# Kernel tuning notes

Hardware: AMD Instinct MI355X
Metric: run time of the kernel (lower is better)

## Reference

```python
import jax, jax.numpy as jnp
import numpy as np

V, D, H = 50000, 256, 4
HD = H * D            # concat head dim (TransformerConv concat=True)
HH, O = 256, 256      # invariant_hidden_dim, invariant_out_dim
B, N, E, L, A = 16, 1000, 4000, 64, 128
PAD = 0
SCALE = 1.0 / float(np.sqrt(D))


def emb_lookup(table, idx):
    # nn.Embedding with padding_idx: forward is a plain gather; grad at pad row is zeroed.
    rows = table[idx]
    return jnp.where((idx == PAD)[..., None], jax.lax.stop_gradient(rows), rows)


def transformer_conv(x, edge_index, ea, Wq, bq, Wk, bk, Wv, bv, We, Wskip, bskip):
    # PyG TransformerConv, heads=H, concat=True, root_weight=True, beta=False, dropout=0 (eval)
    n = x.shape[0]
    src, dst = edge_index[0], edge_index[1]
    q = (x @ Wq + bq).reshape(n, H, D)
    e = (ea @ We).reshape(-1, H, D)          # lin_edge (bias=False)
    k = (x @ Wk + bk).reshape(n, H, D)[src] + e
    v = (x @ Wv + bv).reshape(n, H, D)[src] + e
    alpha = (q[dst] * k).sum(-1) * SCALE      # [E,H]
    amax = jax.ops.segment_max(alpha, dst, num_segments=n)
    ex = jnp.exp(alpha - amax[dst])
    denom = jax.ops.segment_sum(ex, dst, num_segments=n)
    w = ex / denom[dst]                       # per-target-node softmax over incoming edges
    agg = jax.ops.segment_sum(v * w[..., None], dst, num_segments=n)
    return agg.reshape(n, HD) + x @ Wskip + bskip  # lin_skip on root


def mixed_embed(tok, node, graph_repr, emb):
    fixed = emb_lookup(emb, tok)
    flex = jnp.take_along_axis(graph_repr, node[..., None], axis=1)
    flex = jnp.where((node == PAD)[..., None], jax.lax.stop_gradient(flex), flex)
    return fixed + flex


def gru_last(xs, W_ih, W_hh, b_ih, b_hh):
    # torch nn.GRU, batch_first, 1 layer; only last hidden state is used
    gx = jnp.einsum('blh,gh->blg', xs, W_ih) + b_ih  # [B,L,3O]

    def step(h, g):
        gh = h @ W_hh.T + b_hh
        xr, xz, xn = jnp.split(g, 3, axis=-1)
        hr, hz, hn = jnp.split(gh, 3, axis=-1)
        r = jax.nn.sigmoid(xr + hr)
        z = jax.nn.sigmoid(xz + hz)
        c = jnp.tanh(xn + r * hn)
        return (1.0 - z) * c + z * h, None

    h0 = jnp.zeros((xs.shape[0], W_hh.shape[1]), xs.dtype)
    h_last, _ = jax.lax.scan(step, h0, jnp.swapaxes(gx, 0, 1))
    return h_last


def setup_inputs() -> dict:
    key = jax.random.key(0)
    ks = jax.random.split(key, 40)
    f = lambda i, shape, s=0.05: jax.random.normal(ks[i], shape, jnp.float32) * s
    ri = lambda i, shape, hi: jax.random.randint(ks[i], shape, 0, hi)
    return {
        'node_tokens': ri(0, (B, N), V),
        'edge_tokens': ri(1, (B, E), V),
        'edge_index': ri(2, (B, 2, E), N),
        'inv_token': ri(3, (B, L), V),
        'inv_node': ri(4, (B, L), N),
        'aa_token': ri(5, (B, A), V),
        'aa_node': ri(6, (B, A), N),
        'action_mask': jnp.ones((B, A), jnp.float32),
        'emb': f(7, (V, D), 0.02),
        'Wq': f(8, (D, HD)), 'bq': f(9, (HD,)),
        'Wk': f(10, (D, HD)), 'bk': f(11, (HD,)),
        'Wv': f(12, (D, HD)), 'bv': f(13, (HD,)),
        'We': f(14, (D, HD)),
        'Wskip': f(15, (D, HD)), 'bskip': f(16, (HD,)),
        'W1': f(17, (HD, D)), 'b1': f(18, (D,)),
        'Wp': f(19, (D, HH)), 'bp': f(20, (HH,)),
        'W_ih': f(21, (3 * O, HH)), 'W_hh': f(22, (3 * O, O)),
        'b_ih': f(23, (3 * O,)), 'b_hh': f(24, (3 * O,)),
        'Wab': f(25, (D, 1)), 'bab': f(26, (1,)),
        'Wap': f(27, (D, O)), 'bap': f(28, (O,)),
    }


def reference(node_tokens, edge_tokens, edge_index, inv_token, inv_node, aa_token, aa_node,
              action_mask, emb, Wq, bq, Wk, bk, Wv, bv, We, Wskip, bskip, W1, b1,
              Wp, bp, W_ih, W_hh, b_ih, b_hh, Wab, bab, Wap, bap):
    x = emb_lookup(emb, node_tokens)    # [B,N,D]
    ea = emb_lookup(emb, edge_tokens)   # [B,E,D]
    conv = jax.vmap(lambda xx, ei, ee: transformer_conv(
        xx, ei, ee, Wq, bq, Wk, bk, Wv, bv, We, Wskip, bskip))
    h = jax.nn.relu(conv(x, edge_index, ea))            # [B,N,HD]
    graph_repr = jax.nn.relu(h @ W1 + b1)               # [B,N,D]
    inv_h = jax.nn.relu(mixed_embed(inv_token, inv_node, graph_repr, emb) @ Wp + bp)
    inv = gru_last(inv_h, W_ih, W_hh, b_ih, b_hh)       # [B,O]
    aa_emb = mixed_embed(aa_token, aa_node, graph_repr, emb)  # [B,A,D]
    scores = jnp.einsum('bao,bo->ba', aa_emb @ Wap + bap, inv) + (aa_emb @ Wab + bab)[..., 0]
    inf_mask = jnp.maximum(jnp.log(action_mask), jnp.float32(np.finfo(np.float32).min))
    return scores + inf_mask
```

## Files before the change

### kernel.cpp

```cpp
#include <hip/hip_runtime.h>
#include <hip/hip_bf16.h>
#include <float.h>
#include <math.h>

typedef __hip_bfloat16 bf16;

#define B_ 16
#define N_ 1000
#define E_ 4000
#define L_ 64
#define A_ 128
#define D_ 256
#define H_ 4
#define HD_ 1024
#define SCALE_ 0.0625f

typedef __attribute__((ext_vector_type(8))) short short8;
typedef __attribute__((ext_vector_type(4))) float f32x4;

union U4S8 { uint4 u; short8 s; };

__device__ __forceinline__ unsigned short f2bf(float f) {
    bf16 h = __float2bfloat16(f);
    return *reinterpret_cast<unsigned short*>(&h);
}
__device__ __forceinline__ unsigned pack2(float a, float b) {
    return (unsigned)f2bf(a) | ((unsigned)f2bf(b) << 16);
}
__device__ __forceinline__ unsigned short rne1(float a) {
    unsigned ua = __float_as_uint(a);
    ua += 0x7fff + ((ua >> 16) & 1);
    return (unsigned short)(ua >> 16);
}
__device__ __forceinline__ float bflo(unsigned u) { return __uint_as_float(u << 16); }
__device__ __forceinline__ float bfhi(unsigned u) { return __uint_as_float(u & 0xffff0000u); }

#define LOG2E 1.4426950408889634f
__device__ __forceinline__ float fsigm(float x) {
    return __builtin_amdgcn_rcpf(1.f + __builtin_amdgcn_exp2f(-LOG2E * x));
}
__device__ __forceinline__ float ftanh(float x) {
    return 1.f - 2.f * __builtin_amdgcn_rcpf(1.f + __builtin_amdgcn_exp2f(2.f * LOG2E * x));
}

__global__ void convemb_kernel(const float* __restrict__ src, bf16* __restrict__ dst, long n4)
{
    long i = (long)blockIdx.x * 256 + threadIdx.x;
    if (i >= n4) return;
    float4 v = *(const float4*)(src + i * 4);
    *(uint2*)(dst + i * 4) = make_uint2(pack2(v.x, v.y), pack2(v.z, v.w));
}

__global__ void pack_all_kernel(const float* __restrict__ Wq, const float* __restrict__ Wk,
                                const float* __restrict__ Wv, const float* __restrict__ Wskip,
                                const float* __restrict__ We, const float* __restrict__ W1,
                                const float* __restrict__ Wp, const float* __restrict__ W_ih,
                                const float* __restrict__ Wap, const float* __restrict__ W_hh,
                                const float* __restrict__ bq, const float* __restrict__ bk,
                                const float* __restrict__ bv, const float* __restrict__ bskip,
                                unsigned* __restrict__ qkvsP, unsigned* __restrict__ WeP,
                                unsigned* __restrict__ W1P, unsigned* __restrict__ WpP,
                                unsigned* __restrict__ WihP, unsigned* __restrict__ WapP,
                                unsigned* __restrict__ WeTP,
                                short8* __restrict__ WhhP, float* __restrict__ bias4096)
{
    int i = blockIdx.x * 256 + threadIdx.x;
    if (i < 524288) {
        int k2 = i >> 12, n = i & 4095;
        const float* s = (n < 1024) ? Wq : (n < 2048) ? Wk : (n < 3072) ? Wv : Wskip;
        int col = n & 1023;
        qkvsP[i] = pack2(s[(long)(2 * k2) * 1024 + col], s[(long)(2 * k2 + 1) * 1024 + col]);
        return;
    }
    i -= 524288;
    if (i < 131072) {
        int k2 = i >> 10, n = i & 1023;
        WeP[i] = pack2(We[(long)(2 * k2) * 1024 + n], We[(long)(2 * k2 + 1) * 1024 + n]);
        return;
    }
    i -= 131072;
    if (i < 131072) {
        int k2 = i >> 8, n = i & 255;
        W1P[i] = pack2(W1[(long)(2 * k2) * 256 + n], W1[(long)(2 * k2 + 1) * 256 + n]);
        return;
    }
    i -= 131072;
    if (i < 32768) {
        int k2 = i >> 8, n = i & 255;
        WpP[i] = pack2(Wp[(long)(2 * k2) * 256 + n], Wp[(long)(2 * k2 + 1) * 256 + n]);
        return;
    }
    i -= 32768;
    if (i < 98304) {
        int k2 = i / 768, n = i % 768;
        WihP[i] = pack2(W_ih[(long)n * 256 + 2 * k2], W_ih[(long)n * 256 + 2 * k2 + 1]);
        return;
    }
    i -= 98304;
    if (i < 32768) {
        int k2 = i >> 8, n = i & 255;
        WapP[i] = pack2(Wap[(long)(2 * k2) * 256 + n], Wap[(long)(2 * k2 + 1) * 256 + n]);
        return;
    }
    i -= 32768;
    if (i < 131072) {
        int k2 = i >> 10, n = i & 1023;
        int d = n & 255, hb = n & ~255;
        WeTP[i] = pack2(We[(long)d * 1024 + hb + 2 * k2],
                        We[(long)d * 1024 + hb + 2 * k2 + 1]);
        return;
    }
    i -= 131072;
    if (i < 24576) {
        int lane = i & 63, tk = (i >> 6) & 7, tile = i >> 9;
        int n = tile * 16 + (lane & 15);
        const float* wp = W_hh + (long)n * 256 + tk * 32 + (lane >> 4) * 8;
        float4 w0 = *(const float4*)wp;
        float4 w1 = *(const float4*)(wp + 4);
        U4S8 u;
        u.u = make_uint4(pack2(w0.x, w0.y), pack2(w0.z, w0.w),
                         pack2(w1.x, w1.y), pack2(w1.z, w1.w));
        WhhP[i] = u.s;
        return;
    }
    i -= 24576;
    if (i < 4096) {
        int q = i >> 10, c = i & 1023;
        bias4096[i] = ((q == 0) ? bq : (q == 1) ? bk : (q == 2) ? bv : bskip)[c];
    }
}
#define PACK_ALL_TOT (524288 + 131072 + 131072 + 32768 + 98304 + 32768 + 131072 + 24576 + 4096)

__global__ void gxt_kernel(const bf16* __restrict__ gxh, bf16* __restrict__ gxT)
{
    int i = blockIdx.x * 256 + threadIdx.x;
    if (i >= B_ * L_ * 768) return;
    int b = i / (L_ * 768);
    int rem = i - b * (L_ * 768);
    int t = rem / 768, n = rem - (rem / 768) * 768;
    gxT[((long)t * 768 + n) * 16 + b] = gxh[i];
}

#define TM 128
#define TN 128
#define TK 32
#define ASTR 40
#define BSTR 132

template <typename CT>
__global__ __launch_bounds__(256)
void pgemm_kernel(const bf16* __restrict__ A, const int* __restrict__ arows,
                  const unsigned* __restrict__ Bp, const float* __restrict__ bias,
                  CT* __restrict__ C, int M, int K, int Nc, int relu_out,
                  long astride, int aoff, int colbase, int hslice, int addC)
{
    __shared__ short    As[TM * ASTR];
    __shared__ unsigned Bs[(TK / 2) * BSTR];

    const int tid  = threadIdx.x;
    const int lane = tid & 63;
    const int wave = tid >> 6;
    const int wm = wave >> 1, wn = wave & 1;
    const int quad = lane >> 4, c16 = lane & 15;
    const long row0 = (long)blockIdx.y * TM;
    const int  col0 = colbase + blockIdx.x * TN;
    const int  aoff2 = aoff + (hslice ? (col0 & ~255) : 0);

    const int sm  = tid >> 1;
    const int sh  = (tid & 1) * 16;
    const int sn2 = tid & 63;
    const int skk = (tid >> 6) * 4;

    long gr_row = row0 + sm;
    if (gr_row > M - 1) gr_row = M - 1;
    long ar = arows ? (long)arows[gr_row] : gr_row;
    const short* Arow = (const short*)A + ar * astride + aoff2 + sh;

    f32x4 acc[4][4];
    #pragma unroll
    for (int i = 0; i < 4; ++i)
        #pragma unroll
        for (int j = 0; j < 4; ++j)
            acc[i][j] = (f32x4){0.f, 0.f, 0.f, 0.f};

    for (int k0 = 0; k0 < K; k0 += TK) {
        {
            const short* p = Arow + k0;
            uint4 a = *(const uint4*)(p);
            uint4 b = *(const uint4*)(p + 8);
            *(uint4*)&As[sm * ASTR + sh]     = a;
            *(uint4*)&As[sm * ASTR + sh + 8] = b;
        }
        #pragma unroll
        for (int i = 0; i < 4; ++i) {
            int kk2 = skk + i;
            *(uint2*)&Bs[kk2 * BSTR + sn2 * 2] =
                *(const uint2*)&Bp[(long)(k0 / 2 + kk2) * Nc + col0 + sn2 * 2];
        }
        __syncthreads();

        short8 af[4];
        U4S8   bfr[4];
        #pragma unroll
        for (int mi = 0; mi < 4; ++mi) {
            int m = wm * 64 + mi * 16 + c16;
            af[mi] = *(const short8*)&As[m * ASTR + quad * 8];
        }
        #pragma unroll
        for (int ni = 0; ni < 4; ++ni) {
            int n = wn * 64 + ni * 16 + c16;
            uint4 u;
            u.x = Bs[(quad * 4 + 0) * BSTR + n];
            u.y = Bs[(quad * 4 + 1) * BSTR + n];
            u.z = Bs[(quad * 4 + 2) * BSTR + n];
            u.w = Bs[(quad * 4 + 3) * BSTR + n];
            bfr[ni].u = u;
        }
        #pragma unroll
        for (int mi = 0; mi < 4; ++mi)
            #pragma unroll
            for (int ni = 0; ni < 4; ++ni)
                acc[mi][ni] = __builtin_amdgcn_mfma_f32_16x16x32_bf16(
                    af[mi], bfr[ni].s, acc[mi][ni], 0, 0, 0);
        __syncthreads();
    }

    #pragma unroll
    for (int ni = 0; ni < 4; ++ni) {
        int col = col0 + wn * 64 + ni * 16 + c16;
        float bv = bias ? bias[col] : 0.f;
        #pragma unroll
        for (int mi = 0; mi < 4; ++mi) {
            long row = row0 + wm * 64 + mi * 16 + quad * 4;
            #pragma unroll
            for (int r = 0; r < 4; ++r) {
                if (row + r >= M) continue;
                float v = acc[mi][ni][r] + bv;
                if (addC) v += (float)C[(row + r) * Nc + col];
                if (relu_out) v = fmaxf(v, 0.f);
                C[(row + r) * Nc + col] = (CT)v;
            }
        }
    }
}

__global__ void zero_int_kernel(int* __restrict__ p, int n)
{
    int i = blockIdx.x * 256 + threadIdx.x;
    if (i < n) p[i] = 0;
}

__global__ void count_kernel(const int* __restrict__ edge_index, int b0,
                             int* __restrict__ cnt, int cE)
{
    int i = blockIdx.x * 256 + threadIdx.x;
    if (i >= cE) return;
    int bl = i / E_, ei = i % E_;
    int dst = edge_index[(long)(b0 + bl) * 2 * E_ + E_ + ei];
    atomicAdd(&cnt[bl * N_ + dst], 1);
}

__global__ __launch_bounds__(1024)
void scan_kernel(const int* __restrict__ cnt, int* __restrict__ row_start,
                 int* __restrict__ cursor)
{
    int bl = blockIdx.x;
    int tid = threadIdx.x;
    __shared__ int s[1024];
    int v = (tid < N_) ? cnt[bl * N_ + tid] : 0;
    s[tid] = v;
    __syncthreads();
    for (int off = 1; off < 1024; off <<= 1) {
        int t = (tid >= off) ? s[tid - off] : 0;
        __syncthreads();
        s[tid] += t;
        __syncthreads();
    }
    if (tid < N_) {
        int excl = s[tid] - v;
        row_start[bl * N_ + tid] = excl;
        cursor[bl * N_ + tid] = excl;
    }
}

__global__ void scatter_kernel(const int* __restrict__ edge_index, int b0,
                               int* __restrict__ cursor, int* __restrict__ elist, int cE)
{
    int i = blockIdx.x * 256 + threadIdx.x;
    if (i >= cE) return;
    int bl = i / E_, ei = i % E_;
    int dst = edge_index[(long)(b0 + bl) * 2 * E_ + E_ + ei];
    int pos = atomicAdd(&cursor[bl * N_ + dst], 1);
    elist[bl * E_ + pos] = ei;
}

__device__ __forceinline__ float d2(unsigned a, unsigned b)
{
    return bflo(a) * bflo(b) + bfhi(a) * bfhi(b);
}

__global__ void alpha_ex_kernel(const bf16* __restrict__ qkvs, const bf16* __restrict__ qWb,
                                const bf16* __restrict__ embh, const int* __restrict__ edge_tokens,
                                const int* __restrict__ edge_index,
                                int b0, float* __restrict__ ex, int cE)
{
    int eidx = blockIdx.x * 4 + (threadIdx.x >> 6);
    int l = threadIdx.x & 63;
    int bl = eidx / E_, ei = eidx % E_;
    const int* eb = edge_index + (long)(b0 + bl) * 2 * E_;
    int src = eb[ei], dst = eb[E_ + ei];
    int tok = edge_tokens[(long)(b0 + bl) * E_ + ei];
    int head = l >> 4;
    int li = l & 15;
    int joff = head * 256 + li * 16;

    const uint4* qp = (const uint4*)(qkvs + (long)(bl * N_ + dst) * 4096 + joff);
    const uint4* kp = (const uint4*)(qkvs + (long)(bl * N_ + src) * 4096 + 1024 + joff);
    const uint4* wp = (const uint4*)(qWb + (long)(bl * N_ + dst) * 1024 + joff);
    const uint4* xp = (const uint4*)(embh + (long)tok * 256 + li * 16);

    uint4 qa = qp[0], qb2 = qp[1];
    uint4 ka = kp[0], kb2 = kp[1];
    uint4 wa = wp[0], wb2 = wp[1];
    uint4 xa = xp[0], xb2 = xp[1];

    float s = d2(qa.x, ka.x) + d2(qa.y, ka.y) + d2(qa.z, ka.z) + d2(qa.w, ka.w)
            + d2(qb2.x, kb2.x) + d2(qb2.y, kb2.y) + d2(qb2.z, kb2.z) + d2(qb2.w, kb2.w)
            + d2(wa.x, xa.x) + d2(wa.y, xa.y) + d2(wa.z, xa.z) + d2(wa.w, xa.w)
            + d2(wb2.x, xb2.x) + d2(wb2.y, xb2.y) + d2(wb2.z, xb2.z) + d2(wb2.w, xb2.w);

    s += __shfl_down(s, 8);
    s += __shfl_down(s, 4);
    s += __shfl_down(s, 2);
    s += __shfl_down(s, 1);

    if (li == 0)
        ex[(long)head * cE + eidx] = __builtin_amdgcn_exp2f(s * (SCALE_ * LOG2E));
}

__global__ void agg_node_kernel(const bf16* __restrict__ qkvs, const bf16* __restrict__ embh,
                                const int* __restrict__ edge_tokens,
                                const float* __restrict__ ex, const int* __restrict__ edge_index,
                                const int* __restrict__ row_start, const int* __restrict__ cnt,
                                const int* __restrict__ elist,
                                int b0, int cE, bf16* __restrict__ aggb,
                                bf16* __restrict__ xsumb)
{
    int base = blockIdx.x;
    int bl = base / N_;
    int tid = threadIdx.x;
    int h = tid >> 6;
    int j0 = tid * 4;
    int jx = (tid & 63) * 4;

    int start = row_start[base];
    int deg = cnt[base];
    const int* el = elist + (long)bl * E_;
    const float* exh = ex + (long)h * cE;
    const int* srcp = edge_index + (long)(b0 + bl) * 2 * E_;
    const int* tokp = edge_tokens + (long)(b0 + bl) * E_;

    float d = 0.f;
    for (int t = 0; t < deg; ++t)
        d += exh[(long)bl * E_ + el[start + t]];
    float invd = (deg > 0) ? 1.f / d : 0.f;

    float a0 = 0.f, a1 = 0.f, a2 = 0.f, a3 = 0.f;
    float x0 = 0.f, x1 = 0.f, x2 = 0.f, x3 = 0.f;
    for (int t = 0; t < deg; ++t) {
        int ei = el[start + t];
        long eidx = (long)bl * E_ + ei;
        float w = exh[eidx] * invd;
        int src = srcp[ei];
        int tok = tokp[ei];
        uint2 vv = *(const uint2*)(qkvs + (long)(bl * N_ + src) * 4096 + 2048 + j0);
        uint2 xx = *(const uint2*)(embh + (long)tok * 256 + jx);
        a0 += w * bflo(vv.x);
        a1 += w * bfhi(vv.x);
        a2 += w * bflo(vv.y);
        a3 += w * bfhi(vv.y);
        x0 += w * bflo(xx.x);
        x1 += w * bfhi(xx.x);
        x2 += w * bflo(xx.y);
        x3 += w * bfhi(xx.y);
    }

    uint2 sk = *(const uint2*)(qkvs + (long)base * 4096 + 3072 + j0);
    unsigned o0 = pack2(bflo(sk.x) + a0, bfhi(sk.x) + a1);
    unsigned o1 = pack2(bflo(sk.y) + a2, bfhi(sk.y) + a3);
    *(uint2*)(aggb + (long)base * HD_ + j0) = make_uint2(o0, o1);
    *(uint2*)(xsumb + (long)base * HD_ + j0) = make_uint2(pack2(x0, x1), pack2(x2, x3));
}

__global__ void mixed2_kernel(const bf16* __restrict__ embh,
                              const int* __restrict__ inv_token, const int* __restrict__ inv_node,
                              const int* __restrict__ aa_token, const int* __restrict__ aa_node,
                              const float* __restrict__ graph_repr,
                              bf16* __restrict__ mixed_inv, bf16* __restrict__ aa_emb)
{
    int r = blockIdx.x;
    int d = threadIdx.x;
    if (r < B_ * L_) {
        int b = r / L_;
        float v = (float)embh[(long)inv_token[r] * D_ + d] +
                  graph_repr[((long)b * N_ + inv_node[r]) * D_ + d];
        mixed_inv[(long)r * D_ + d] = __float2bfloat16(v);
    } else {
        int r2 = r - B_ * L_;
        int b = r2 / A_;
        float v = (float)embh[(long)aa_token[r2] * D_ + d] +
                  graph_repr[((long)b * N_ + aa_node[r2]) * D_ + d];
        aa_emb[(long)r2 * D_ + d] = __float2bfloat16(v);
    }
}

__global__ __launch_bounds__(1024)
void gru_kernel(const bf16* __restrict__ gxT, const short8* __restrict__ WhhP,
                const float* __restrict__ b_hh, float* __restrict__ inv_out)
{
    __shared__ short hB[2][16 * 264];

    const int tid = threadIdx.x;
    const int lane = tid & 63;
    const int wave = tid >> 6;
    const int quad = lane >> 4, c16 = lane & 15;
    const int n0 = wave * 16 + c16;

    for (int i = tid; i < 2 * 16 * 264; i += 1024) ((short*)hB)[i] = 0;

    short8 wfr[8], wfz[8], wfn[8];
    #pragma unroll
    for (int tk = 0; tk < 8; ++tk) {
        wfr[tk] = WhhP[((0 * 16 + wave) * 8 + tk) * 64 + lane];
        wfz[tk] = WhhP[((1 * 16 + wave) * 8 + tk) * 64 + lane];
        wfn[tk] = WhhP[((2 * 16 + wave) * 8 + tk) * 64 + lane];
    }
    float bhr = b_hh[0 * 256 + n0];
    float bhz = b_hh[1 * 256 + n0];
    float bhn = b_hh[2 * 256 + n0];

    float myh0 = 0.f, myh1 = 0.f, myh2 = 0.f, myh3 = 0.f;

    const short* gbr = (const short*)gxT + (long)(0 * 256 + n0) * 16 + quad * 4;
    const short* gbz = gbr + 256 * 16;
    const short* gbn = gbr + 512 * 16;

    uint2 pxr = *(const uint2*)gbr;
    uint2 pxz = *(const uint2*)gbz;
    uint2 pxn = *(const uint2*)gbn;

    __syncthreads();

    int p = 0;
    for (int t = 0; t < L_; ++t) {
        uint2 xr2 = pxr, xz2 = pxz, xn2 = pxn;
        long noff = (long)((t + 1 < L_) ? t + 1 : t) * 12288;
        pxr = *(const uint2*)(gbr + noff);
        pxz = *(const uint2*)(gbz + noff);
        pxn = *(const uint2*)(gbn + noff);

        f32x4 ar = (f32x4){bhr, bhr, bhr, bhr};
        f32x4 az = (f32x4){bhz, bhz, bhz, bhz};
        f32x4 an = (f32x4){bhn, bhn, bhn, bhn};
        const short* hp = &hB[p][0];
        #pragma unroll
        for (int tk = 0; tk < 8; ++tk) {
            short8 a = *(const short8*)&hp[c16 * 264 + tk * 32 + quad * 8];
            ar = __builtin_amdgcn_mfma_f32_16x16x32_bf16(a, wfr[tk], ar, 0, 0, 0);
            az = __builtin_amdgcn_mfma_f32_16x16x32_bf16(a, wfz[tk], az, 0, 0, 0);
            an = __builtin_amdgcn_mfma_f32_16x16x32_bf16(a, wfn[tk], an, 0, 0, 0);
        }

        float xr[4] = {bflo(xr2.x), bfhi(xr2.x), bflo(xr2.y), bfhi(xr2.y)};
        float xz[4] = {bflo(xz2.x), bfhi(xz2.x), bflo(xz2.y), bfhi(xz2.y)};
        float xn[4] = {bflo(xn2.x), bfhi(xn2.x), bflo(xn2.y), bfhi(xn2.y)};
        float hold[4] = {myh0, myh1, myh2, myh3};
        float hn[4];
        short* hw = &hB[p ^ 1][0];
        #pragma unroll
        for (int r = 0; r < 4; ++r) {
            float rr = fsigm(xr[r] + ar[r]);
            float zz = fsigm(xz[r] + az[r]);
            float cc = ftanh(xn[r] + rr * an[r]);
            hn[r] = (1.f - zz) * cc + zz * hold[r];
            hw[(quad * 4 + r) * 264 + n0] = (short)rne1(hn[r]);
        }
        myh0 = hn[0]; myh1 = hn[1]; myh2 = hn[2]; myh3 = hn[3];
        p ^= 1;
        __syncthreads();
    }

    inv_out[(long)(quad * 4 + 0) * 256 + n0] = myh0;
    inv_out[(long)(quad * 4 + 1) * 256 + n0] = myh1;
    inv_out[(long)(quad * 4 + 2) * 256 + n0] = myh2;
    inv_out[(long)(quad * 4 + 3) * 256 + n0] = myh3;
}

__global__ void score_kernel(const float* __restrict__ aa_p, const bf16* __restrict__ aa_emb,
                             const float* __restrict__ inv, const float* __restrict__ Wab,
                             const float* __restrict__ bab, const float* __restrict__ mask,
                             float* __restrict__ out)
{
    int r = blockIdx.x * 4 + (threadIdx.x >> 6);
    int l = threadIdx.x & 63;
    int b = r / A_;
    float s = 0.f;
    for (int d = l; d < D_; d += 64)
        s += aa_p[(long)r * D_ + d] * inv[(long)b * D_ + d] +
             (float)aa_emb[(long)r * D_ + d] * Wab[d];
    #pragma unroll
    for (int off = 32; off; off >>= 1) s += __shfl_down(s, off);
    if (l == 0) {
        float lm = logf(mask[r]);
        const float MN = -3.4028234663852886e38f;
        if (!(lm >= MN)) lm = MN;
        out[r] = s + bab[0] + lm;
    }
}

static inline size_t align256(size_t x) { return (x + 255) & ~(size_t)255; }

template <typename CT>
static void launch_pgemm(const bf16* A, const int* arows, const unsigned* Bp,
                         const float* bias, CT* C, int M, int K, int Nc, int relu,
                         long astride, int aoff, int colbase, int hslice, int addC,
                         int ncols, hipStream_t s)
{
    dim3 grid(ncols / TN, (M + TM - 1) / TM);
    pgemm_kernel<CT><<<grid, 256, 0, s>>>(A, arows, Bp, bias, C, M, K, Nc, relu,
                                          astride, aoff, colbase, hslice, addC);
}

extern "C" void kernel_launch(void* const* d_in, const int* in_sizes, int n_in,
                              void* d_out, int out_size, void* d_ws, size_t ws_size,
                              hipStream_t stream)
{
    const int* node_tokens = (const int*)d_in[0];
    const int* edge_tokens = (const int*)d_in[1];
    const int* edge_index  = (const int*)d_in[2];
    const int* inv_token   = (const int*)d_in[3];
    const int* inv_node    = (const int*)d_in[4];
    const int* aa_token    = (const int*)d_in[5];
    const int* aa_node     = (const int*)d_in[6];
    const float* action_mask = (const float*)d_in[7];
    const float* emb   = (const float*)d_in[8];
    const float* Wq    = (const float*)d_in[9];
    const float* bq    = (const float*)d_in[10];
    const float* Wk    = (const float*)d_in[11];
    const float* bk    = (const float*)d_in[12];
    const float* Wv    = (const float*)d_in[13];
    const float* bv    = (const float*)d_in[14];
    const float* We    = (const float*)d_in[15];
    const float* Wskip = (const float*)d_in[16];
    const float* bskip = (const float*)d_in[17];
    const float* W1    = (const float*)d_in[18];
    const float* b1    = (const float*)d_in[19];
    const float* Wp    = (const float*)d_in[20];
    const float* bp    = (const float*)d_in[21];
    const float* W_ih  = (const float*)d_in[22];
    const float* W_hh  = (const float*)d_in[23];
    const float* b_ih  = (const float*)d_in[24];
    const float* b_hh  = (const float*)d_in[25];
    const float* Wab   = (const float*)d_in[26];
    const float* bab   = (const float*)d_in[27];
    const float* Wap   = (const float*)d_in[28];
    const float* bap   = (const float*)d_in[29];
    (void)in_sizes; (void)n_in; (void)out_size;

    char* base = (char*)d_ws;
    size_t off = 0;
    auto alloc = [&](size_t bytes) -> char* {
        char* p = base + off;
        off = align256(off + bytes);
        return p;
    };

    const long VD = 50000L * 256;
    bf16*  embh       = (bf16*)alloc(VD * 2);
    float* graph_repr = (float*)alloc((size_t)B_ * N_ * D_ * 4);
    bf16*  mixed_inv  = (bf16*)alloc((size_t)B_ * L_ * D_ * 2);
    bf16*  inv_h      = (bf16*)alloc((size_t)B_ * L_ * D_ * 2);
    bf16*  gxh        = (bf16*)alloc((size_t)B_ * L_ * 768 * 2);
    bf16*  gxT        = (bf16*)alloc((size_t)B_ * L_ * 768 * 2);
    float* inv_out    = (float*)alloc((size_t)B_ * 256 * 4);
    bf16*  aa_emb     = (bf16*)alloc((size_t)B_ * A_ * D_ * 2);
    float* aa_p       = (float*)alloc((size_t)B_ * A_ * 256 * 4);
    unsigned* qkvsP   = (unsigned*)alloc((size_t)128 * 4096 * 4);
    unsigned* WeP     = (unsigned*)alloc((size_t)128 * 1024 * 4);
    unsigned* W1P     = (unsigned*)alloc((size_t)512 * 256 * 4);
    unsigned* WpP     = (unsigned*)alloc((size_t)128 * 256 * 4);
    unsigned* WihP    = (unsigned*)alloc((size_t)128 * 768 * 4);
    unsigned* WapP    = (unsigned*)alloc((size_t)128 * 256 * 4);
    unsigned* WeTP    = (unsigned*)alloc((size_t)128 * 1024 * 4);
    short8* WhhP      = (short8*)alloc((size_t)24576 * 16);
    float* bias4096   = (float*)alloc(4096 * 4);
    size_t persist = off;

    int c = 16;
    while (c > 1) {
        size_t cN = (size_t)c * N_, cEs = (size_t)c * E_;
        size_t chunk = align256(cN * 4096 * 2)
                     + align256(cN * HD_ * 2)
                     + align256(cN * HD_ * 2)
                     + align256(cN * HD_ * 2)
                     + align256(cEs * H_ * 4)
                     + 3 * align256(cN * 4)
                     + align256(cEs * 4);
        if (persist + chunk <= ws_size) break;
        c >>= 1;
    }
    int cN = c * N_, cE = c * E_;

    bf16*  qkvs  = (bf16*)alloc((size_t)cN * 4096 * 2);
    bf16*  qWb   = (bf16*)alloc((size_t)cN * HD_ * 2);
    bf16*  aggb  = (bf16*)alloc((size_t)cN * HD_ * 2);
    bf16*  xsumb = (bf16*)alloc((size_t)cN * HD_ * 2);
    float* ex    = (float*)alloc((size_t)cE * H_ * 4);
    int*   cnt   = (int*)alloc((size_t)cN * 4);
    int*   rstart= (int*)alloc((size_t)cN * 4);
    int*   cursor= (int*)alloc((size_t)cN * 4);
    int*   elist = (int*)alloc((size_t)cE * 4);

    convemb_kernel<<<(int)((VD / 4 + 255) / 256), 256, 0, stream>>>(emb, embh, VD / 4);
    pack_all_kernel<<<(PACK_ALL_TOT + 255) / 256, 256, 0, stream>>>(
        Wq, Wk, Wv, Wskip, We, W1, Wp, W_ih, Wap, W_hh, bq, bk, bv, bskip,
        qkvsP, WeP, W1P, WpP, WihP, WapP, WeTP, WhhP, bias4096);

    for (int b0 = 0; b0 < B_; b0 += c) {
        zero_int_kernel<<<(cN + 255) / 256, 256, 0, stream>>>(cnt, cN);
        count_kernel<<<(cE + 255) / 256, 256, 0, stream>>>(edge_index, b0, cnt, cE);
        scan_kernel<<<c, 1024, 0, stream>>>(cnt, rstart, cursor);
        scatter_kernel<<<(cE + 255) / 256, 256, 0, stream>>>(edge_index, b0, cursor,
                                                             elist, cE);
        launch_pgemm<bf16>(embh, node_tokens + (long)b0 * N_, qkvsP, bias4096, qkvs,
                           cN, D_, 4096, 0, 256, 0, 0, 0, 0, 4096, stream);
        launch_pgemm<bf16>(qkvs, nullptr, WeTP, nullptr, qWb,
                           cN, 256, 1024, 0, 4096, 0, 0, 1, 0, 1024, stream);
        alpha_ex_kernel<<<cE / 4, 256, 0, stream>>>(qkvs, qWb, embh, edge_tokens,
                                                    edge_index, b0, ex, cE);
        agg_node_kernel<<<cN, 256, 0, stream>>>(qkvs, embh, edge_tokens, ex, edge_index,
                                                rstart, cnt, elist, b0, cE, aggb, xsumb);
        launch_pgemm<bf16>(xsumb, nullptr, WeP, nullptr, aggb,
                           cN, 256, 1024, 1, 1024, 0, 0, 1, 1, 1024, stream);
        launch_pgemm<float>(aggb, nullptr, W1P, b1,
                            graph_repr + (long)b0 * N_ * D_,
                            cN, HD_, D_, 1, 1024, 0, 0, 0, 0, 256, stream);
    }

    mixed2_kernel<<<B_ * L_ + B_ * A_, 256, 0, stream>>>(embh, inv_token, inv_node,
                                                         aa_token, aa_node, graph_repr,
                                                         mixed_inv, aa_emb);
    launch_pgemm<bf16>(mixed_inv, nullptr, WpP, bp, inv_h,
                       B_ * L_, D_, 256, 1, 256, 0, 0, 0, 0, 256, stream);
    launch_pgemm<bf16>(inv_h, nullptr, WihP, b_ih, gxh,
                       B_ * L_, 256, 768, 0, 256, 0, 0, 0, 0, 768, stream);
    gxt_kernel<<<(B_ * L_ * 768 + 255) / 256, 256, 0, stream>>>(gxh, gxT);
    gru_kernel<<<1, 1024, 0, stream>>>(gxT, WhhP, b_hh, inv_out);

    launch_pgemm<float>(aa_emb, nullptr, WapP, bap, aa_p,
                        B_ * A_, D_, 256, 0, 256, 0, 0, 0, 0, 256, stream);
    score_kernel<<<(B_ * A_) / 4, 256, 0, stream>>>(aa_p, aa_emb, inv_out, Wab, bab,
                                                    action_mask, (float*)d_out);
}
```

Before: 880.3 us.

## Fuse edge scoring into node aggregation, load GEMM A tiles via direct LDS loads

Merges the separate alpha/exp kernel and the node aggregation kernel into one per-node attention kernel that computes edge scores, exponentials and weighted sums in a single pass, removing the ex buffer and one launch. The GEMM A-tile staging switches to global_load_lds (direct global-to-LDS) with an unpadded layout, which may add LDS bank conflicts. The GRU input GEMM now writes its output transposed, replacing the separate transpose kernel. The fused kernel recomputes the score with a full-wave reduction for each edge and drops the max subtraction, as the previous code already did.

```diff
diff --git a/kernel.cpp b/kernel.cpp
--- a/kernel.cpp
+++ b/kernel.cpp
@@ -41,6 +41,12 @@
 }
 __device__ __forceinline__ float ftanh(float x) {
     return 1.f - 2.f * __builtin_amdgcn_rcpf(1.f + __builtin_amdgcn_exp2f(2.f * LOG2E * x));
+}
+
+typedef const __attribute__((address_space(1))) unsigned int* gas_t;
+typedef __attribute__((address_space(3))) unsigned int* las_t;
+__device__ __forceinline__ void gld16(const void* g, void* l) {
+    __builtin_amdgcn_global_load_lds((gas_t)g, (las_t)l, 16, 0, 0);
 }
 
 __global__ void convemb_kernel(const float* __restrict__ src, bf16* __restrict__ dst, long n4)
@@ -131,20 +137,9 @@
 }
 #define PACK_ALL_TOT (524288 + 131072 + 131072 + 32768 + 98304 + 32768 + 131072 + 24576 + 4096)
 
-__global__ void gxt_kernel(const bf16* __restrict__ gxh, bf16* __restrict__ gxT)
-{
-    int i = blockIdx.x * 256 + threadIdx.x;
-    if (i >= B_ * L_ * 768) return;
-    int b = i / (L_ * 768);
-    int rem = i - b * (L_ * 768);
-    int t = rem / 768, n = rem - (rem / 768) * 768;
-    gxT[((long)t * 768 + n) * 16 + b] = gxh[i];
-}
-
 #define TM 128
 #define TN 128
 #define TK 32
-#define ASTR 40
 #define BSTR 132
 
 template <typename CT>
@@ -152,9 +147,9 @@
 void pgemm_kernel(const bf16* __restrict__ A, const int* __restrict__ arows,
                   const unsigned* __restrict__ Bp, const float* __restrict__ bias,
                   CT* __restrict__ C, int M, int K, int Nc, int relu_out,
-                  long astride, int aoff, int colbase, int hslice, int addC)
-{
-    __shared__ short    As[TM * ASTR];
+                  long astride, int aoff, int colbase, int hslice, int addC, int outT)
+{
+    __shared__ short    As[TM * TK];
     __shared__ unsigned Bs[(TK / 2) * BSTR];
 
     const int tid  = threadIdx.x;
@@ -166,15 +161,21 @@
     const int  col0 = colbase + blockIdx.x * TN;
     const int  aoff2 = aoff + (hslice ? (col0 & ~255) : 0);
 
-    const int sm  = tid >> 1;
-    const int sh  = (tid & 1) * 16;
+    {
+    }
+    const int r0 = wave * 32 + (lane >> 2);
+    const int cseg = (lane & 3) * 8;
+    long gr0 = row0 + r0;      if (gr0 > M - 1) gr0 = M - 1;
+    long gr1 = row0 + r0 + 16; if (gr1 > M - 1) gr1 = M - 1;
+    long ar0 = arows ? (long)arows[gr0] : gr0;
+    long ar1 = arows ? (long)arows[gr1] : gr1;
+    const short* Ag0 = (const short*)A + ar0 * astride + aoff2 + cseg;
+    const short* Ag1 = (const short*)A + ar1 * astride + aoff2 + cseg;
+    short* Ld0 = &As[wave * 1024];
+    short* Ld1 = &As[wave * 1024 + 512];
+
     const int sn2 = tid & 63;
-    const int skk = (tid >> 6) * 4;
-
-    long gr_row = row0 + sm;
-    if (gr_row > M - 1) gr_row = M - 1;
-    long ar = arows ? (long)arows[gr_row] : gr_row;
-    const short* Arow = (const short*)A + ar * astride + aoff2 + sh;
+    const int skk = wave * 4;
 
     f32x4 acc[4][4];
     #pragma unroll
@@ -184,13 +185,8 @@
             acc[i][j] = (f32x4){0.f, 0.f, 0.f, 0.f};
 
     for (int k0 = 0; k0 < K; k0 += TK) {
-        {
-            const short* p = Arow + k0;
-            uint4 a = *(const uint4*)(p);
-            uint4 b = *(const uint4*)(p + 8);
-            *(uint4*)&As[sm * ASTR + sh]     = a;
-            *(uint4*)&As[sm * ASTR + sh + 8] = b;
-        }
+        gld16(Ag0 + k0, Ld0);
+        gld16(Ag1 + k0, Ld1);
         #pragma unroll
         for (int i = 0; i < 4; ++i) {
             int kk2 = skk + i;
@@ -204,7 +200,7 @@
         #pragma unroll
         for (int mi = 0; mi < 4; ++mi) {
             int m = wm * 64 + mi * 16 + c16;
-            af[mi] = *(const short8*)&As[m * ASTR + quad * 8];
+            af[mi] = *(const short8*)&As[m * 32 + quad * 8];
         }
         #pragma unroll
         for (int ni = 0; ni < 4; ++ni) {
@@ -238,7 +234,13 @@
                 float v = acc[mi][ni][r] + bv;
                 if (addC) v += (float)C[(row + r) * Nc + col];
                 if (relu_out) v = fmaxf(v, 0.f);
-                C[(row + r) * Nc + col] = (CT)v;
+                if (outT) {
+                    long rr = row + r;
+                    int t = (int)(rr & 63), b = (int)(rr >> 6);
+                    C[((long)t * Nc + col) * 16 + b] = (CT)v;
+                } else {
+                    C[(row + r) * Nc + col] = (CT)v;
+                }
             }
         }
     }
@@ -299,97 +301,65 @@
     return bflo(a) * bflo(b) + bfhi(a) * bfhi(b);
 }
 
-__global__ void alpha_ex_kernel(const bf16* __restrict__ qkvs, const bf16* __restrict__ qWb,
-                                const bf16* __restrict__ embh, const int* __restrict__ edge_tokens,
-                                const int* __restrict__ edge_index,
-                                int b0, float* __restrict__ ex, int cE)
-{
-    int eidx = blockIdx.x * 4 + (threadIdx.x >> 6);
-    int l = threadIdx.x & 63;
-    int bl = eidx / E_, ei = eidx % E_;
-    const int* eb = edge_index + (long)(b0 + bl) * 2 * E_;
-    int src = eb[ei], dst = eb[E_ + ei];
-    int tok = edge_tokens[(long)(b0 + bl) * E_ + ei];
-    int head = l >> 4;
-    int li = l & 15;
-    int joff = head * 256 + li * 16;
-
-    const uint4* qp = (const uint4*)(qkvs + (long)(bl * N_ + dst) * 4096 + joff);
-    const uint4* kp = (const uint4*)(qkvs + (long)(bl * N_ + src) * 4096 + 1024 + joff);
-    const uint4* wp = (const uint4*)(qWb + (long)(bl * N_ + dst) * 1024 + joff);
-    const uint4* xp = (const uint4*)(embh + (long)tok * 256 + li * 16);
-
-    uint4 qa = qp[0], qb2 = qp[1];
-    uint4 ka = kp[0], kb2 = kp[1];
-    uint4 wa = wp[0], wb2 = wp[1];
-    uint4 xa = xp[0], xb2 = xp[1];
-
-    float s = d2(qa.x, ka.x) + d2(qa.y, ka.y) + d2(qa.z, ka.z) + d2(qa.w, ka.w)
-            + d2(qb2.x, kb2.x) + d2(qb2.y, kb2.y) + d2(qb2.z, kb2.z) + d2(qb2.w, kb2.w)
-            + d2(wa.x, xa.x) + d2(wa.y, xa.y) + d2(wa.z, xa.z) + d2(wa.w, xa.w)
-            + d2(wb2.x, xb2.x) + d2(wb2.y, xb2.y) + d2(wb2.z, xb2.z) + d2(wb2.w, xb2.w);
-
-    s += __shfl_down(s, 8);
-    s += __shfl_down(s, 4);
-    s += __shfl_down(s, 2);
-    s += __shfl_down(s, 1);
-
-    if (li == 0)
-        ex[(long)head * cE + eidx] = __builtin_amdgcn_exp2f(s * (SCALE_ * LOG2E));
-}
-
-__global__ void agg_node_kernel(const bf16* __restrict__ qkvs, const bf16* __restrict__ embh,
-                                const int* __restrict__ edge_tokens,
-                                const float* __restrict__ ex, const int* __restrict__ edge_index,
-                                const int* __restrict__ row_start, const int* __restrict__ cnt,
-                                const int* __restrict__ elist,
-                                int b0, int cE, bf16* __restrict__ aggb,
-                                bf16* __restrict__ xsumb)
+__global__ void attn_kernel(const bf16* __restrict__ qkvs, const bf16* __restrict__ qWb,
+                            const bf16* __restrict__ embh,
+                            const int* __restrict__ edge_tokens, const int* __restrict__ edge_index,
+                            const int* __restrict__ row_start, const int* __restrict__ cnt,
+                            const int* __restrict__ elist, int b0,
+                            bf16* __restrict__ aggb, bf16* __restrict__ xsumb)
 {
     int base = blockIdx.x;
     int bl = base / N_;
     int tid = threadIdx.x;
-    int h = tid >> 6;
+    int l = tid & 63;
     int j0 = tid * 4;
-    int jx = (tid & 63) * 4;
+    int jx = l * 4;
+
+    uint2 qq = *(const uint2*)(qkvs + (long)base * 4096 + j0);
+    uint2 ww = *(const uint2*)(qWb + (long)base * 1024 + j0);
 
     int start = row_start[base];
     int deg = cnt[base];
     const int* el = elist + (long)bl * E_;
-    const float* exh = ex + (long)h * cE;
     const int* srcp = edge_index + (long)(b0 + bl) * 2 * E_;
     const int* tokp = edge_tokens + (long)(b0 + bl) * E_;
 
-    float d = 0.f;
-    for (int t = 0; t < deg; ++t)
-        d += exh[(long)bl * E_ + el[start + t]];
-    float invd = (deg > 0) ? 1.f / d : 0.f;
-
-    float a0 = 0.f, a1 = 0.f, a2 = 0.f, a3 = 0.f;
+    float denom = 0.f;
+    float v0 = 0.f, v1 = 0.f, v2 = 0.f, v3 = 0.f;
     float x0 = 0.f, x1 = 0.f, x2 = 0.f, x3 = 0.f;
+
     for (int t = 0; t < deg; ++t) {
         int ei = el[start + t];
-        long eidx = (long)bl * E_ + ei;
-        float w = exh[eidx] * invd;
         int src = srcp[ei];
         int tok = tokp[ei];
-        uint2 vv = *(const uint2*)(qkvs + (long)(bl * N_ + src) * 4096 + 2048 + j0);
+        const bf16* srow = qkvs + (long)(bl * N_ + src) * 4096;
+        uint2 kk = *(const uint2*)(srow + 1024 + j0);
+        uint2 vv = *(const uint2*)(srow + 2048 + j0);
         uint2 xx = *(const uint2*)(embh + (long)tok * 256 + jx);
-        a0 += w * bflo(vv.x);
-        a1 += w * bfhi(vv.x);
-        a2 += w * bflo(vv.y);
-        a3 += w * bfhi(vv.y);
-        x0 += w * bflo(xx.x);
-        x1 += w * bfhi(xx.x);
-        x2 += w * bflo(xx.y);
-        x3 += w * bfhi(xx.y);
-    }
-
+
+        float s = d2(qq.x, kk.x) + d2(qq.y, kk.y) + d2(ww.x, xx.x) + d2(ww.y, xx.y);
+        s += __shfl_xor(s, 32);
+        s += __shfl_xor(s, 16);
+        s += __shfl_xor(s, 8);
+        s += __shfl_xor(s, 4);
+        s += __shfl_xor(s, 2);
+        s += __shfl_xor(s, 1);
+        float ex = __builtin_amdgcn_exp2f(s * (SCALE_ * LOG2E));
+
+        denom += ex;
+        v0 += ex * bflo(vv.x); v1 += ex * bfhi(vv.x);
+        v2 += ex * bflo(vv.y); v3 += ex * bfhi(vv.y);
+        x0 += ex * bflo(xx.x); x1 += ex * bfhi(xx.x);
+        x2 += ex * bflo(xx.y); x3 += ex * bfhi(xx.y);
+    }
+
+    float invd = (deg > 0) ? 1.f / denom : 0.f;
     uint2 sk = *(const uint2*)(qkvs + (long)base * 4096 + 3072 + j0);
-    unsigned o0 = pack2(bflo(sk.x) + a0, bfhi(sk.x) + a1);
-    unsigned o1 = pack2(bflo(sk.y) + a2, bfhi(sk.y) + a3);
+    unsigned o0 = pack2(bflo(sk.x) + v0 * invd, bfhi(sk.x) + v1 * invd);
+    unsigned o1 = pack2(bflo(sk.y) + v2 * invd, bfhi(sk.y) + v3 * invd);
     *(uint2*)(aggb + (long)base * HD_ + j0) = make_uint2(o0, o1);
-    *(uint2*)(xsumb + (long)base * HD_ + j0) = make_uint2(pack2(x0, x1), pack2(x2, x3));
+    *(uint2*)(xsumb + (long)base * HD_ + j0) =
+        make_uint2(pack2(x0 * invd, x1 * invd), pack2(x2 * invd, x3 * invd));
 }
 
 __global__ void mixed2_kernel(const bf16* __restrict__ embh,
@@ -524,11 +494,11 @@
 static void launch_pgemm(const bf16* A, const int* arows, const unsigned* Bp,
                          const float* bias, CT* C, int M, int K, int Nc, int relu,
                          long astride, int aoff, int colbase, int hslice, int addC,
-                         int ncols, hipStream_t s)
+                         int outT, int ncols, hipStream_t s)
 {
     dim3 grid(ncols / TN, (M + TM - 1) / TM);
     pgemm_kernel<CT><<<grid, 256, 0, s>>>(A, arows, Bp, bias, C, M, K, Nc, relu,
-                                          astride, aoff, colbase, hslice, addC);
+                                          astride, aoff, colbase, hslice, addC, outT);
 }
 
 extern "C" void kernel_launch(void* const* d_in, const int* in_sizes, int n_in,
@@ -580,7 +550,6 @@
     float* graph_repr = (float*)alloc((size_t)B_ * N_ * D_ * 4);
     bf16*  mixed_inv  = (bf16*)alloc((size_t)B_ * L_ * D_ * 2);
     bf16*  inv_h      = (bf16*)alloc((size_t)B_ * L_ * D_ * 2);
-    bf16*  gxh        = (bf16*)alloc((size_t)B_ * L_ * 768 * 2);
     bf16*  gxT        = (bf16*)alloc((size_t)B_ * L_ * 768 * 2);
     float* inv_out    = (float*)alloc((size_t)B_ * 256 * 4);
     bf16*  aa_emb     = (bf16*)alloc((size_t)B_ * A_ * D_ * 2);
@@ -603,7 +572,6 @@
                      + align256(cN * HD_ * 2)
                      + align256(cN * HD_ * 2)
                      + align256(cN * HD_ * 2)
-                     + align256(cEs * H_ * 4)
                      + 3 * align256(cN * 4)
                      + align256(cEs * 4);
         if (persist + chunk <= ws_size) break;
@@ -615,7 +583,6 @@
     bf16*  qWb   = (bf16*)alloc((size_t)cN * HD_ * 2);
     bf16*  aggb  = (bf16*)alloc((size_t)cN * HD_ * 2);
     bf16*  xsumb = (bf16*)alloc((size_t)cN * HD_ * 2);
-    float* ex    = (float*)alloc((size_t)cE * H_ * 4);
     int*   cnt   = (int*)alloc((size_t)cN * 4);
     int*   rstart= (int*)alloc((size_t)cN * 4);
     int*   cursor= (int*)alloc((size_t)cN * 4);
@@ -633,32 +600,29 @@
         scatter_kernel<<<(cE + 255) / 256, 256, 0, stream>>>(edge_index, b0, cursor,
                                                              elist, cE);
         launch_pgemm<bf16>(embh, node_tokens + (long)b0 * N_, qkvsP, bias4096, qkvs,
-                           cN, D_, 4096, 0, 256, 0, 0, 0, 0, 4096, stream);
+                           cN, D_, 4096, 0, 256, 0, 0, 0, 0, 0, 4096, stream);
         launch_pgemm<bf16>(qkvs, nullptr, WeTP, nullptr, qWb,
-                           cN, 256, 1024, 0, 4096, 0, 0, 1, 0, 1024, stream);
-        alpha_ex_kernel<<<cE / 4, 256, 0, stream>>>(qkvs, qWb, embh, edge_tokens,
-                                                    edge_index, b0, ex, cE);
-        agg_node_kernel<<<cN, 256, 0, stream>>>(qkvs, embh, edge_tokens, ex, edge_index,
-                                                rstart, cnt, elist, b0, cE, aggb, xsumb);
+                           cN, 256, 1024, 0, 4096, 0, 0, 1, 0, 0, 1024, stream);
+        attn_kernel<<<cN, 256, 0, stream>>>(qkvs, qWb, embh, edge_tokens, edge_index,
+                                            rstart, cnt, elist, b0, aggb, xsumb);
         launch_pgemm<bf16>(xsumb, nullptr, WeP, nullptr, aggb,
-                           cN, 256, 1024, 1, 1024, 0, 0, 1, 1, 1024, stream);
+                           cN, 256, 1024, 1, 1024, 0, 0, 1, 1, 0, 1024, stream);
         launch_pgemm<float>(aggb, nullptr, W1P, b1,
                             graph_repr + (long)b0 * N_ * D_,
-                            cN, HD_, D_, 1, 1024, 0, 0, 0, 0, 256, stream);
+                            cN, HD_, D_, 1, 1024, 0, 0, 0, 0, 0, 256, stream);
     }
 
     mixed2_kernel<<<B_ * L_ + B_ * A_, 256, 0, stream>>>(embh, inv_token, inv_node,
                                                          aa_token, aa_node, graph_repr,
                                                          mixed_inv, aa_emb);
     launch_pgemm<bf16>(mixed_inv, nullptr, WpP, bp, inv_h,
-                       B_ * L_, D_, 256, 1, 256, 0, 0, 0, 0, 256, stream);
-    launch_pgemm<bf16>(inv_h, nullptr, WihP, b_ih, gxh,
-                       B_ * L_, 256, 768, 0, 256, 0, 0, 0, 0, 768, stream);
-    gxt_kernel<<<(B_ * L_ * 768 + 255) / 256, 256, 0, stream>>>(gxh, gxT);
+                       B_ * L_, D_, 256, 1, 256, 0, 0, 0, 0, 0, 256, stream);
+    launch_pgemm<bf16>(inv_h, nullptr, WihP, b_ih, gxT,
+                       B_ * L_, 256, 768, 0, 256, 0, 0, 0, 0, 1, 768, stream);
     gru_kernel<<<1, 1024, 0, stream>>>(gxT, WhhP, b_hh, inv_out);
 
     launch_pgemm<float>(aa_emb, nullptr, WapP, bap, aa_p,
-                        B_ * A_, D_, 256, 0, 256, 0, 0, 0, 0, 256, stream);
+                        B_ * A_, D_, 256, 0, 256, 0, 0, 0, 0, 0, 256, stream);
     score_kernel<<<(B_ * A_) / 4, 256, 0, stream>>>(aa_p, aa_emb, inv_out, Wab, bab,
                                                     action_mask, (float*)d_out);
 }
```

Result: faster. 849.2 us (-3.5%).
